# Kernel tuning notes

Measured on AMD Instinct MI355X. Metric: run time of the kernel, lower is better.

## Reference

```python
import jax, jax.numpy as jnp
import numpy as np
import math

N_EMBD = 1024
N_HEAD = 16
B, T = 2, 2048
MASK_VAL = -10.0  # non-standard soft mask value from original module


def setup_inputs() -> dict:
    key = jax.random.key(0)
    k1, k2, k3 = jax.random.split(key, 3)
    scale = 1.0 / math.sqrt(N_EMBD)
    x = jax.random.normal(k1, (B, T, N_EMBD), dtype=jnp.float32)
    # torch Linear weights: (out_features, in_features)
    w_attn = jax.random.normal(k2, (3 * N_EMBD, N_EMBD), dtype=jnp.float32) * scale
    w_proj = jax.random.normal(k3, (N_EMBD, N_EMBD), dtype=jnp.float32) * scale
    return {"x": x, "w_attn": w_attn, "w_proj": w_proj}


def reference(x, w_attn, w_proj):
    Bsz, Tlen, C = x.shape
    hs = C // N_HEAD
    qkv = jnp.einsum('btc,fc->btf', x, w_attn)  # [B,T,3C]
    q, k, v = jnp.split(qkv, 3, axis=-1)
    # [B,H,T,hs]
    q = q.reshape(Bsz, Tlen, N_HEAD, hs).transpose(0, 2, 1, 3)
    k = k.reshape(Bsz, Tlen, N_HEAD, hs).transpose(0, 2, 1, 3)
    v = v.reshape(Bsz, Tlen, N_HEAD, hs).transpose(0, 2, 1, 3)
    att = jnp.einsum('bhqd,bhkd->bhqk', q, k) * (1.0 / math.sqrt(hs))
    causal = jnp.tril(jnp.ones((Tlen, Tlen), dtype=bool))
    att = jnp.where(causal[None, None], att, MASK_VAL)
    att = jax.nn.softmax(att, axis=-1)
    y = jnp.einsum('bhqk,bhkd->bhqd', att, v)
    y = y.transpose(0, 2, 1, 3).reshape(Bsz, Tlen, C)
    return jnp.einsum('btc,fc->btf', y, w_proj)
```

## Files before the change

kernel.cpp:

```cpp
#include <hip/hip_runtime.h>
#include <hip/hip_bf16.h>
#include <stdint.h>

#define BSZ   2
#define TT    2048
#define NH    16
#define HS    64
#define CC    1024
#define C3    3072
#define MT    4096
#define E10   4.5399929762484854e-05f
#define SCL2  0.1803368801111204f

typedef __bf16 bf16;
typedef __bf16 bf16x8 __attribute__((ext_vector_type(8)));
typedef float  f32x4  __attribute__((ext_vector_type(4)));
typedef short  s16x4  __attribute__((ext_vector_type(4)));

#define AS1 __attribute__((address_space(1)))
#define AS3 __attribute__((address_space(3)))

__device__ __forceinline__ void glds16(const bf16* g, bf16* l) {
    __builtin_amdgcn_global_load_lds((const AS1 void*)g, (AS3 void*)l, 16, 0, 0);
}

__global__ void detect_dtype(const uint16_t* __restrict__ x, int* __restrict__ flag) {
    __shared__ int cnt;
    if (threadIdx.x == 0) cnt = 0;
    __syncthreads();
    int local = 0;
    for (int i = threadIdx.x; i < 512; i += 256) {
        uint16_t u = x[i];
        int e = (u >> 7) & 0xFF;
        if (e >= 96 && e <= 159) local++;
    }
    atomicAdd(&cnt, local);
    __syncthreads();
    if (threadIdx.x == 0) *flag = (cnt >= 461) ? 0 : 1;
}

#define NX8  (MT * CC / 8)
#define NWA8 (C3 * CC / 8)
#define NWP8 (CC * CC / 8)
__global__ __launch_bounds__(256)
void convert_all(const float* __restrict__ x, const float* __restrict__ wa,
                 const float* __restrict__ wp, bf16* __restrict__ xd,
                 bf16* __restrict__ wad, bf16* __restrict__ wpd,
                 const int* __restrict__ flag) {
    if (*flag == 0) return;
    long i = (long)blockIdx.x * 256 + threadIdx.x;
    const float* s; bf16* d; long off;
    if (i < NX8)             { s = x;  d = xd;  off = i; }
    else if (i < NX8 + NWA8) { s = wa; d = wad; off = i - NX8; }
    else                     { s = wp; d = wpd; off = i - NX8 - NWA8; }
    const float4* sp = reinterpret_cast<const float4*>(s) + off * 2;
    float4 a = sp[0], b = sp[1];
    bf16x8 r;
    r[0] = (bf16)a.x; r[1] = (bf16)a.y; r[2] = (bf16)a.z; r[3] = (bf16)a.w;
    r[4] = (bf16)b.x; r[5] = (bf16)b.y; r[6] = (bf16)b.z; r[7] = (bf16)b.w;
    reinterpret_cast<bf16x8*>(d)[off] = r;
}

__global__ __launch_bounds__(256)
void gemm_bt(const bf16* __restrict__ A0, const bf16* __restrict__ A1,
             const bf16* __restrict__ B0, const bf16* __restrict__ B1,
             void* __restrict__ Cmain, bf16* __restrict__ Cv,
             const int* __restrict__ flag,
             int M, int N, int K, int lda, int ldb, int ldc,
             int split_col, int cf32_dyn) {
    __shared__ bf16 As[2][128 * 32];
    __shared__ bf16 Bs[2][128 * 32];

    const int f = *flag;
    const bf16* A = f ? A1 : A0;
    const bf16* B = f ? B1 : B0;
    const int cf32 = cf32_dyn & f;

    const int tid  = threadIdx.x;
    const int lane = tid & 63;
    const int wave = tid >> 6;
    const int wm   = wave >> 1;
    const int wn   = wave & 1;
    const int quad = lane >> 4;
    const int l16  = lane & 15;

    const int row0 = blockIdx.y * 128;
    const int col0 = blockIdx.x * 128;

    const int srow = tid >> 2;
    const int skk  = (tid & 3) * 8;

    const bf16* Ap = A + (long)(row0 + srow) * lda + skk;
    const bf16* Bp = B + (long)(col0 + srow) * ldb + skk;

    auto stage = [&](int k0, int buf) {
        glds16(Ap + k0,                  &As[buf][wave * 512]);
        glds16(Ap + (long)64 * lda + k0, &As[buf][wave * 512 + 2048]);
        glds16(Bp + k0,                  &Bs[buf][wave * 512]);
        glds16(Bp + (long)64 * ldb + k0, &Bs[buf][wave * 512 + 2048]);
    };

    f32x4 acc[4][4] = {};
    stage(0, 0);

    for (int k0 = 0; k0 < K; k0 += 32) {
        const int buf = (k0 >> 5) & 1;
        __syncthreads();
        if (k0 + 32 < K) stage(k0 + 32, buf ^ 1);

        const bf16* Ac = As[buf];
        const bf16* Bc = Bs[buf];
        bf16x8 af[4], bfv[4];
#pragma unroll
        for (int mi = 0; mi < 4; ++mi)
            af[mi] = *reinterpret_cast<const bf16x8*>(&Ac[(wm * 64 + mi * 16 + l16) * 32 + quad * 8]);
#pragma unroll
        for (int ni = 0; ni < 4; ++ni)
            bfv[ni] = *reinterpret_cast<const bf16x8*>(&Bc[(wn * 64 + ni * 16 + l16) * 32 + quad * 8]);
#pragma unroll
        for (int mi = 0; mi < 4; ++mi)
#pragma unroll
            for (int ni = 0; ni < 4; ++ni)
                acc[mi][ni] = __builtin_amdgcn_mfma_f32_16x16x32_bf16(af[mi], bfv[ni], acc[mi][ni], 0, 0, 0);
    }

    if (split_col < 0 || col0 < split_col) {
#pragma unroll
        for (int mi = 0; mi < 4; ++mi)
#pragma unroll
            for (int ni = 0; ni < 4; ++ni)
#pragma unroll
                for (int r = 0; r < 4; ++r) {
                    int row = row0 + wm * 64 + mi * 16 + quad * 4 + r;
                    int col = col0 + wn * 64 + ni * 16 + l16;
                    float v = acc[mi][ni][r];
                    if (cf32) ((float*)Cmain)[(long)row * ldc + col] = v;
                    else      ((bf16*)Cmain)[(long)row * ldc + col] = (bf16)v;
                }
    } else {
        const int h  = (col0 - split_col + wn * 64) >> 6;
        const int bq = row0 >> 11;
        const int tc = ((row0 & 2047) >> 6) + wm;
#pragma unroll
        for (int ni = 0; ni < 4; ++ni) {
            long vrow = (long)(bq * NH + h) * 64 + ni * 16 + l16;
#pragma unroll
            for (int mi = 0; mi < 4; ++mi) {
                bf16 outv[4];
#pragma unroll
                for (int r = 0; r < 4; ++r) outv[r] = (bf16)acc[mi][ni][r];
                *reinterpret_cast<uint2*>(&Cv[vrow * 2048 + tc * 64 + quad * 16 + mi * 4]) =
                    *reinterpret_cast<uint2*>(outv);
            }
        }
    }
}

__global__ __launch_bounds__(256)
void gemm_bt64(const bf16* __restrict__ A0, const bf16* __restrict__ A1,
               const bf16* __restrict__ B0, const bf16* __restrict__ B1,
               void* __restrict__ C, const int* __restrict__ flag,
               int M, int N, int K, int lda, int ldb, int ldc, int cf32_dyn) {
    __shared__ bf16 As[2][128 * 32];
    __shared__ bf16 Bs[2][64 * 32];

    const int f = *flag;
    const bf16* A = f ? A1 : A0;
    const bf16* B = f ? B1 : B0;
    const int cf32 = cf32_dyn & f;

    const int tid  = threadIdx.x;
    const int lane = tid & 63;
    const int wave = tid >> 6;
    const int wm   = wave >> 1;
    const int wn   = wave & 1;
    const int quad = lane >> 4;
    const int l16  = lane & 15;

    const int row0 = blockIdx.y * 128;
    const int col0 = blockIdx.x * 64;

    const int srow = tid >> 2;
    const int skk  = (tid & 3) * 8;

    const bf16* Ap = A + (long)(row0 + srow) * lda + skk;
    const bf16* Bp = B + (long)(col0 + srow) * ldb + skk;

    auto stage = [&](int k0, int buf) {
        glds16(Ap + k0,                  &As[buf][wave * 512]);
        glds16(Ap + (long)64 * lda + k0, &As[buf][wave * 512 + 2048]);
        glds16(Bp + k0,                  &Bs[buf][wave * 512]);
    };

    f32x4 acc[4][2] = {};
    stage(0, 0);

    for (int k0 = 0; k0 < K; k0 += 32) {
        const int buf = (k0 >> 5) & 1;
        __syncthreads();
        if (k0 + 32 < K) stage(k0 + 32, buf ^ 1);

        const bf16* Ac = As[buf];
        const bf16* Bc = Bs[buf];
        bf16x8 af[4], bfv[2];
#pragma unroll
        for (int mi = 0; mi < 4; ++mi)
            af[mi] = *reinterpret_cast<const bf16x8*>(&Ac[(wm * 64 + mi * 16 + l16) * 32 + quad * 8]);
#pragma unroll
        for (int ni = 0; ni < 2; ++ni)
            bfv[ni] = *reinterpret_cast<const bf16x8*>(&Bc[(wn * 32 + ni * 16 + l16) * 32 + quad * 8]);
#pragma unroll
        for (int mi = 0; mi < 4; ++mi)
#pragma unroll
            for (int ni = 0; ni < 2; ++ni)
                acc[mi][ni] = __builtin_amdgcn_mfma_f32_16x16x32_bf16(af[mi], bfv[ni], acc[mi][ni], 0, 0, 0);
    }

#pragma unroll
    for (int mi = 0; mi < 4; ++mi)
#pragma unroll
        for (int ni = 0; ni < 2; ++ni)
#pragma unroll
            for (int r = 0; r < 4; ++r) {
                int row = row0 + wm * 64 + mi * 16 + quad * 4 + r;
                int col = col0 + wn * 32 + ni * 16 + l16;
                float v = acc[mi][ni][r];
                if (cf32) ((float*)C)[(long)row * ldc + col] = v;
                else      ((bf16*)C)[(long)row * ldc + col] = (bf16)v;
            }
}

__global__ __launch_bounds__(256)
void vtile2(const bf16* __restrict__ Vt, float* __restrict__ Vtile) {
    const int kt = blockIdx.x, bh = blockIdx.y;
    const int tid = threadIdx.x;
    const int d = tid >> 2, part = tid & 3;
    const bf16* p = Vt + ((long)bh * 64 + d) * 2048 + kt * 64 + part * 16;
    float s = 0.f;
#pragma unroll
    for (int i = 0; i < 2; ++i) {
        bf16x8 v = *reinterpret_cast<const bf16x8*>(p + i * 8);
#pragma unroll
        for (int j = 0; j < 8; ++j) s += (float)v[j];
    }
    s += __shfl_xor(s, 1, 64);
    s += __shfl_xor(s, 2, 64);
    if (part == 0) Vtile[((long)bh * 32 + kt) * 64 + d] = s;
}

__global__ void vts_suffix(const float* __restrict__ Vtile, float* __restrict__ Vts) {
    const int bh = blockIdx.x, d = threadIdx.x;
    Vts[((long)bh * 33 + 32) * 64 + d] = 0.f;
    float acc = 0.f;
    for (int kt = 31; kt >= 0; --kt) {
        acc += Vtile[((long)bh * 32 + kt) * 64 + d];
        Vts[((long)bh * 33 + kt) * 64 + d] = acc;
    }
}

__global__ __launch_bounds__(256)
void attn(bf16* __restrict__ qk, const bf16* __restrict__ Vt,
          const float* __restrict__ Vts) {
    __shared__ bf16 Ks[2][64 * 64];
    __shared__ bf16 Vs[2][64 * 64];

    const int tid  = threadIdx.x;
    const int lane = tid & 63;
    const int wave = tid >> 6;
    const int quad = lane >> 4;
    const int l16  = lane & 15;

    const int f2   = blockIdx.x;
    const int xcd  = f2 & 7;
    const int slot = f2 >> 3;
    const int bh   = (slot & 3) * 8 + xcd;
    const int chunk = 31 - (slot >> 2);
    const int b = bh >> 4, h = bh & 15;
    const int q0 = chunk * 64;
    const long rbase = (long)b * TT;

    const bf16* qp = qk + (rbase + q0 + wave * 16 + l16) * 2048 + h * HS;
    bf16x8 qf0 = *reinterpret_cast<const bf16x8*>(qp + quad * 8);
    bf16x8 qf1 = *reinterpret_cast<const bf16x8*>(qp + 32 + quad * 8);

    f32x4 O[4] = {};
    float lp = 0.f;

    const int rl  = lane >> 3;
    const int cs  = (lane & 7) ^ rl;
    const int row0dma = wave * 16 + rl;
    const bf16* kgb = qk + (rbase + row0dma) * 2048 + CC + h * HS + cs * 8;
    const bf16* vgb = Vt + ((long)(b * NH + h) * 64 + row0dma) * 2048 + cs * 8;
    const int sx = l16 & 7;

    auto stage = [&](int kt, int buf) {
        glds16(kgb + (long)(kt * 64) * 2048,     &Ks[buf][wave * 1024]);
        glds16(kgb + (long)(kt * 64 + 8) * 2048, &Ks[buf][wave * 1024 + 512]);
        glds16(vgb + kt * 64,                    &Vs[buf][wave * 1024]);
        glds16(vgb + 8 * 2048 + kt * 64,         &Vs[buf][wave * 1024 + 512]);
    };

    const int ktend = chunk + 1;
    stage(0, 0);

    for (int kt = 0; kt < ktend; ++kt) {
        const int buf = kt & 1;
        __syncthreads();
        if (kt + 1 < ktend) stage(kt + 1, buf ^ 1);

        const bf16* Kc = Ks[buf];
        const bf16* Vc = Vs[buf];

        bf16x8 kf0[4], kf1[4];
#pragma unroll
        for (int g = 0; g < 4; ++g) {
            const int krow = g * 16 + l16;
            kf0[g] = *reinterpret_cast<const bf16x8*>(&Kc[krow * 64 + ((quad ^ sx) * 8)]);
            kf1[g] = *reinterpret_cast<const bf16x8*>(&Kc[krow * 64 + (((4 + quad) ^ sx) * 8)]);
        }
        s16x4 vf[4][4];
#pragma unroll
        for (int dg = 0; dg < 4; ++dg) {
            const int vrow = dg * 16 + l16;
            union { uint4 u; s16x4 s[2]; } ua, ub;
            ua.u = *reinterpret_cast<const uint4*>(&Vc[vrow * 64 + (((2 * quad) ^ sx) * 8)]);
            ub.u = *reinterpret_cast<const uint4*>(&Vc[vrow * 64 + (((2 * quad + 1) ^ sx) * 8)]);
            vf[dg][0] = ua.s[0]; vf[dg][1] = ua.s[1];
            vf[dg][2] = ub.s[0]; vf[dg][3] = ub.s[1];
        }

        f32x4 S[4] = {};
#pragma unroll
        for (int g = 0; g < 4; ++g) {
            S[g] = __builtin_amdgcn_mfma_f32_16x16x32_bf16(kf0[g], qf0, S[g], 0, 0, 0);
            S[g] = __builtin_amdgcn_mfma_f32_16x16x32_bf16(kf1[g], qf1, S[g], 0, 0, 0);
        }

        const bool dtile = (kt == chunk);
        const int ql = wave * 16 + l16;
        s16x4 pk[4];
#pragma unroll
        for (int g = 0; g < 4; ++g) {
#pragma unroll
            for (int r = 0; r < 4; ++r) {
                float p = __builtin_exp2f(S[g][r] * SCL2);
                if (dtile) {
                    int kl = g * 16 + quad * 4 + r;
                    p = (kl > ql) ? E10 : p;
                }
                lp += p;
                union { bf16 b_; short s_; } u;
                u.b_ = (bf16)p;
                pk[g][r] = u.s_;
            }
        }

#pragma unroll
        for (int dg = 0; dg < 4; ++dg) {
            O[dg] = __builtin_amdgcn_mfma_f32_16x16x16bf16_1k(vf[dg][0], pk[0], O[dg], 0, 0, 0);
            O[dg] = __builtin_amdgcn_mfma_f32_16x16x16bf16_1k(vf[dg][1], pk[1], O[dg], 0, 0, 0);
            O[dg] = __builtin_amdgcn_mfma_f32_16x16x16bf16_1k(vf[dg][2], pk[2], O[dg], 0, 0, 0);
            O[dg] = __builtin_amdgcn_mfma_f32_16x16x16bf16_1k(vf[dg][3], pk[3], O[dg], 0, 0, 0);
        }
    }

    lp += __shfl_xor(lp, 16, 64);
    lp += __shfl_xor(lp, 32, 64);

    const int nfut = TT - ktend * 64;
    const float l = lp + (float)nfut * E10;
    const float invl = 1.0f / l;
    const float* vfp = Vts + ((long)(b * NH + h) * 33 + ktend) * 64;

    bf16* yp = qk + (rbase + q0 + wave * 16 + l16) * 2048 + h * HS;
#pragma unroll
    for (int dg = 0; dg < 4; ++dg) {
        bf16 outv[4];
#pragma unroll
        for (int r = 0; r < 4; ++r) {
            float o = O[dg][r] + E10 * vfp[dg * 16 + quad * 4 + r];
            outv[r] = (bf16)(o * invl);
        }
        *reinterpret_cast<uint2*>(yp + dg * 16 + quad * 4) =
            *reinterpret_cast<uint2*>(outv);
    }
}

extern "C" void kernel_launch(void* const* d_in, const int* in_sizes, int n_in,
                              void* d_out, int out_size, void* d_ws, size_t ws_size,
                              hipStream_t stream) {
    const void* x      = d_in[0];
    const void* w_attn = d_in[1];
    const void* w_proj = d_in[2];

    char* ws = (char*)d_ws;
    bf16*  qk     = (bf16*)ws;
    bf16*  Vt     = (bf16*)(ws + (size_t)MT * 2048 * 2);
    char*  p2     = ws + (size_t)MT * 2048 * 2 + (size_t)32 * 64 * 2048 * 2;
    int*   flag   = (int*)p2;
    float* Vts    = (float*)(p2 + 256);
    bf16*  wp_cvt = (bf16*)(p2 + 256 + 32 * 33 * 64 * 4);
    float* Vtile  = (float*)((char*)wp_cvt + (size_t)CC * CC * 2);

    bf16* x_cvt  = (bf16*)d_out;
    bf16* wa_cvt = (bf16*)d_out + (size_t)MT * CC;

    detect_dtype<<<1, 256, 0, stream>>>((const uint16_t*)x, flag);
    convert_all<<<(NX8 + NWA8 + NWP8) / 256, 256, 0, stream>>>(
        (const float*)x, (const float*)w_attn, (const float*)w_proj,
        x_cvt, wa_cvt, wp_cvt, flag);

    gemm_bt<<<dim3(C3 / 128, MT / 128), 256, 0, stream>>>(
        (const bf16*)x, x_cvt, (const bf16*)w_attn, wa_cvt, qk, Vt, flag,
        MT, C3, CC, CC, CC, 2048, 2048, 0);

    vtile2<<<dim3(32, BSZ * NH), 256, 0, stream>>>(Vt, Vtile);
    vts_suffix<<<dim3(BSZ * NH), dim3(64), 0, stream>>>(Vtile, Vts);

    attn<<<dim3(1024), 256, 0, stream>>>(qk, Vt, Vts);

    gemm_bt64<<<dim3(CC / 64, MT / 128), 256, 0, stream>>>(
        qk, qk, (const bf16*)w_proj, wp_cvt, d_out, flag,
        MT, CC, CC, 2048, CC, CC, 1);
}
```

Measured before the change: 182.0 us.

## Split attention KV range into segments and add a combine kernel

Splits each query chunk's key range into up to four segments of eight key tiles each, launching 2560 blocks instead of 1024 to balance the causal workload. Chunks that span more than one segment write fp32 partial outputs and row sums to a workspace, and a new combine kernel sums them, adds the masked-future contribution and normalizes. Because the softmax has no max subtraction, partials combine by plain addition. The cost is extra global traffic for the partials, one more launch, and more workspace.

```diff
diff --git a/kernel.cpp b/kernel.cpp
--- a/kernel.cpp
+++ b/kernel.cpp
@@ -260,7 +260,8 @@
 
 __global__ __launch_bounds__(256)
 void attn(bf16* __restrict__ qk, const bf16* __restrict__ Vt,
-          const float* __restrict__ Vts) {
+          const float* __restrict__ Vts, float* __restrict__ Opart,
+          float* __restrict__ Lpart) {
     __shared__ bf16 Ks[2][64 * 64];
     __shared__ bf16 Vs[2][64 * 64];
 
@@ -274,10 +275,19 @@
     const int xcd  = f2 & 7;
     const int slot = f2 >> 3;
     const int bh   = (slot & 3) * 8 + xcd;
-    const int chunk = 31 - (slot >> 2);
+    const int sid  = slot >> 2;
+    int seg, chunk;
+    if      (sid < 32) { seg = 0; chunk = 31 - sid; }
+    else if (sid < 56) { seg = 1; chunk = 31 - (sid - 32); }
+    else if (sid < 72) { seg = 2; chunk = 31 - (sid - 56); }
+    else               { seg = 3; chunk = 31 - (sid - 72); }
+
     const int b = bh >> 4, h = bh & 15;
     const int q0 = chunk * 64;
     const long rbase = (long)b * TT;
+    const int ktfull = chunk + 1;
+    const int kbeg = seg * 8;
+    const int kend = (kbeg + 8 < ktfull) ? (kbeg + 8) : ktfull;
 
     const bf16* qp = qk + (rbase + q0 + wave * 16 + l16) * 2048 + h * HS;
     bf16x8 qf0 = *reinterpret_cast<const bf16x8*>(qp + quad * 8);
@@ -300,13 +310,12 @@
         glds16(vgb + 8 * 2048 + kt * 64,         &Vs[buf][wave * 1024 + 512]);
     };
 
-    const int ktend = chunk + 1;
-    stage(0, 0);
-
-    for (int kt = 0; kt < ktend; ++kt) {
+    stage(kbeg, 0);
+
+    for (int kt = kbeg; kt < kend; ++kt) {
         const int buf = kt & 1;
         __syncthreads();
-        if (kt + 1 < ktend) stage(kt + 1, buf ^ 1);
+        if (kt + 1 < kend) stage(kt + 1, buf ^ 1);
 
         const bf16* Kc = Ks[buf];
         const bf16* Vc = Vs[buf];
@@ -367,23 +376,78 @@
     lp += __shfl_xor(lp, 16, 64);
     lp += __shfl_xor(lp, 32, 64);
 
+    const int q = wave * 16 + l16;
+
+    if (chunk < 8) {
+        const int nfut = TT - ktfull * 64;
+        const float l = lp + (float)nfut * E10;
+        const float invl = 1.0f / l;
+        const float* vfp = Vts + ((long)bh * 33 + ktfull) * 64;
+
+        bf16* yp = qk + (rbase + q0 + q) * 2048 + h * HS;
+#pragma unroll
+        for (int dg = 0; dg < 4; ++dg) {
+            bf16 outv[4];
+#pragma unroll
+            for (int r = 0; r < 4; ++r) {
+                float o = O[dg][r] + E10 * vfp[dg * 16 + quad * 4 + r];
+                outv[r] = (bf16)(o * invl);
+            }
+            *reinterpret_cast<uint2*>(yp + dg * 16 + quad * 4) =
+                *reinterpret_cast<uint2*>(outv);
+        }
+    } else {
+        const long pslot = (long)bh * 80 + sid;
+        float* Op = Opart + pslot * 4096 + q * 64;
+#pragma unroll
+        for (int dg = 0; dg < 4; ++dg)
+            *reinterpret_cast<f32x4*>(Op + dg * 16 + quad * 4) = O[dg];
+        if (quad == 0) Lpart[pslot * 64 + q] = lp;
+    }
+}
+
+__global__ __launch_bounds__(256)
+void attn_combine(const float* __restrict__ Opart, const float* __restrict__ Lpart,
+                  const float* __restrict__ Vts, bf16* __restrict__ qk) {
+    const int c  = 8 + blockIdx.x;
+    const int bh = blockIdx.y;
+    const int b = bh >> 4, h = bh & 15;
+    const int nseg = (c < 16) ? 2 : (c < 24) ? 3 : 4;
+    const int t = threadIdx.x;
+    const int q  = t >> 2;
+    const int dq = (t & 3) * 16;
+
+    f32x4 of[4] = {};
+    float lp = 0.f;
+#pragma unroll
+    for (int s = 0; s < 4; ++s) {
+        if (s < nseg) {
+            const int sb = (s == 0) ? 0 : (s == 1) ? 32 : (s == 2) ? 56 : 72;
+            const long slot = (long)bh * 80 + sb + (31 - c);
+            const float* Op = Opart + slot * 4096 + q * 64 + dq;
+#pragma unroll
+            for (int j = 0; j < 4; ++j)
+                of[j] += *reinterpret_cast<const f32x4*>(Op + j * 4);
+            lp += Lpart[slot * 64 + q];
+        }
+    }
+
+    const int ktend = c + 1;
     const int nfut = TT - ktend * 64;
     const float l = lp + (float)nfut * E10;
     const float invl = 1.0f / l;
-    const float* vfp = Vts + ((long)(b * NH + h) * 33 + ktend) * 64;
-
-    bf16* yp = qk + (rbase + q0 + wave * 16 + l16) * 2048 + h * HS;
-#pragma unroll
-    for (int dg = 0; dg < 4; ++dg) {
-        bf16 outv[4];
-#pragma unroll
-        for (int r = 0; r < 4; ++r) {
-            float o = O[dg][r] + E10 * vfp[dg * 16 + quad * 4 + r];
-            outv[r] = (bf16)(o * invl);
-        }
-        *reinterpret_cast<uint2*>(yp + dg * 16 + quad * 4) =
-            *reinterpret_cast<uint2*>(outv);
-    }
+    const float* vfp = Vts + ((long)bh * 33 + ktend) * 64 + dq;
+
+    bf16 outv[16];
+#pragma unroll
+    for (int j = 0; j < 4; ++j)
+#pragma unroll
+        for (int r = 0; r < 4; ++r)
+            outv[j * 4 + r] = (bf16)((of[j][r] + E10 * vfp[j * 4 + r]) * invl);
+
+    bf16* yp = qk + ((long)b * TT + c * 64 + q) * 2048 + h * HS + dq;
+    *reinterpret_cast<uint4*>(yp)     = *reinterpret_cast<uint4*>(&outv[0]);
+    *reinterpret_cast<uint4*>(yp + 8) = *reinterpret_cast<uint4*>(&outv[8]);
 }
 
 extern "C" void kernel_launch(void* const* d_in, const int* in_sizes, int n_in,
@@ -401,6 +465,9 @@
     float* Vts    = (float*)(p2 + 256);
     bf16*  wp_cvt = (bf16*)(p2 + 256 + 32 * 33 * 64 * 4);
     float* Vtile  = (float*)((char*)wp_cvt + (size_t)CC * CC * 2);
+    char*  p3     = (char*)Vtile + 32 * 32 * 64 * 4;
+    float* Opart  = (float*)p3;
+    float* Lpart  = (float*)(p3 + (size_t)2560 * 4096 * 4);
 
     bf16* x_cvt  = (bf16*)d_out;
     bf16* wa_cvt = (bf16*)d_out + (size_t)MT * CC;
@@ -417,7 +484,8 @@
     vtile2<<<dim3(32, BSZ * NH), 256, 0, stream>>>(Vt, Vtile);
     vts_suffix<<<dim3(BSZ * NH), dim3(64), 0, stream>>>(Vtile, Vts);
 
-    attn<<<dim3(1024), 256, 0, stream>>>(qk, Vt, Vts);
+    attn<<<dim3(2560), 256, 0, stream>>>(qk, Vt, Vts, Opart, Lpart);
+    attn_combine<<<dim3(24, 32), 256, 0, stream>>>(Opart, Lpart, Vts, qk);
 
     gemm_bt64<<<dim3(CC / 64, MT / 128), 256, 0, stream>>>(
         qk, qk, (const bf16*)w_proj, wp_cvt, d_out, flag,
```

New measurement: 193.5 us. 1.06x slower.
